# Optimization experiments

Measured on AMD Instinct MI355X. Metric: run time of the kernel, lower is better.

Reference implementation:

```python
import jax
import jax.numpy as jnp
from jax import lax
import numpy as np

EPS = 1e-5
CLASS_COUNT = 1000

# conv specs: (out_c, in_c, k, pool_stride)
_SPECS = [(8, 1, 11, 1), (32, 8, 7, 2), (64, 32, 5, 2), (64, 64, 5, 2), (128, 64, 5, 2), (128, 128, 3, 2)]


def _maxpool3(x, stride):
    return lax.reduce_window(x, -jnp.inf, lax.max, (1, 1, 3, 3), (1, 1, stride, stride), 'VALID')


def _block(x, w, gamma, beta, pool_stride):
    # tanh soft-binarized weights (mode=1, w=1)
    wq = jnp.tanh(w)
    y = lax.conv_general_dilated(x, wq, (1, 1), 'VALID', dimension_numbers=('NCHW', 'OIHW', 'NCHW'))
    y = _maxpool3(y, pool_stride)
    # BatchNorm2d in training mode: batch statistics over (N,H,W), biased var
    mu = jnp.mean(y, axis=(0, 2, 3), keepdims=True)
    var = jnp.var(y, axis=(0, 2, 3), keepdims=True)
    y = (y - mu) * lax.rsqrt(var + EPS)
    y = y * gamma.reshape(1, -1, 1, 1) + beta.reshape(1, -1, 1, 1)
    # tanh soft-binarized activation (mode=1, w=1)
    return jnp.tanh(y)


def setup_inputs() -> dict:
    key = jax.random.key(0)
    keys = jax.random.split(key, 8)
    inp = {'x': jax.random.normal(keys[0], (128, 1, 227, 227), dtype=jnp.float32)}
    for i, (oc, ic, k, _) in enumerate(_SPECS):
        fan_in = ic * k * k
        inp[f'w{i+1}'] = jax.random.normal(keys[i + 1], (oc, ic, k, k), dtype=jnp.float32) / np.sqrt(fan_in)
        inp[f'g{i+1}'] = jnp.ones((oc,), dtype=jnp.float32)
        inp[f'b{i+1}'] = jnp.zeros((oc,), dtype=jnp.float32)
    inp['wl'] = jax.random.normal(keys[7], (CLASS_COUNT, 512), dtype=jnp.float32) / np.sqrt(512.0)
    return inp


def reference(x, w1, w2, w3, w4, w5, w6, g1, g2, g3, g4, g5, g6,
              b1, b2, b3, b4, b5, b6, wl):
    ws = (w1, w2, w3, w4, w5, w6)
    gs = (g1, g2, g3, g4, g5, g6)
    bs = (b1, b2, b3, b4, b5, b6)
    for i, (_, _, _, ps) in enumerate(_SPECS):
        x = _block(x, ws[i], gs[i], bs[i], ps)
    # flatten -> BinaryLinear (tanh-binarized weight, no bias)
    x = x.reshape(x.shape[0], -1)  # [B, 512]
    return x @ jnp.tanh(wl).T  # [B, classCount]
```

## Files before the change

### kernel.cpp

```cpp
#include <hip/hip_runtime.h>
#include <hip/hip_bf16.h>
#include <hip/hip_fp16.h>

using bf16 = __hip_bfloat16;
using f16  = _Float16;
using f16x8 = __attribute__((ext_vector_type(8))) _Float16;
using f32x4  = __attribute__((ext_vector_type(4))) float;
typedef unsigned long long u64;

__device__ __forceinline__ float b2f(bf16 v){ return __bfloat162float(v); }
__device__ __forceinline__ bf16 f2b(float v){ return __float2bfloat16(v); }
__device__ __forceinline__ float ldf(const float* p){ return *p; }
__device__ __forceinline__ float ldf(const bf16* p){ return b2f(*p); }
__device__ __forceinline__ float ldf(const __half* p){ return __half2float(*p); }
__device__ __forceinline__ void stf(float* p, float v){ *p = v; }
__device__ __forceinline__ void stf(bf16* p, float v){ *p = f2b(v); }
__device__ __forceinline__ void stf(__half* p, float v){ *p = __float2half(v); }

__global__ void detect_dtype(const void* __restrict__ g1, int* __restrict__ flag)
{
    if (blockIdx.x == 0 && threadIdx.x == 0)
        *flag = (*(const unsigned*)g1 == 0x3F803F80u) ? 1 : 0;
}

__device__ __forceinline__ float ld_any(const void* p, int i, int isBf16)
{
    return isBf16 ? b2f(((const bf16*)p)[i]) : ((const float*)p)[i];
}

__global__ void xconv(const void* __restrict__ xin, float* __restrict__ xf,
                      const int* __restrict__ flag, int n)
{
    int bf = *flag;
    int i = blockIdx.x * blockDim.x + threadIdx.x;
    if (i < n) xf[i] = ld_any(xin, i, bf);
}

__global__ void wq_tanh(const void* __restrict__ w, float* __restrict__ wq,
                        const int* __restrict__ flag, int n)
{
    int bf = *flag;
    int i = blockIdx.x * blockDim.x + threadIdx.x;
    if (i < n) wq[i] = tanhf(ld_any(w, i, bf));
}

__global__ void wl_transform(const void* __restrict__ wl, float* __restrict__ wlqT,
                             const int* __restrict__ flag)
{
    int bf = *flag;
    int i = blockIdx.x * blockDim.x + threadIdx.x;
    if (i < 1000 * 512) {
        int cls = i >> 9;
        int k   = i & 511;
        wlqT[k * 1000 + cls] = tanhf(ld_any(wl, i, bf));
    }
}

__global__ void wprep_b2(const void* __restrict__ w2, const int* __restrict__ flag,
                         __half* __restrict__ wpk)
{
    int bf = *flag;
    int i = blockIdx.x * 256 + threadIdx.x;
    if (i >= 13728) return;
    int pair = i / 264;
    int slot = i - pair * 264;
    __half v = __float2half(0.f);
    if (pair < 49 && slot < 256) {
        int oc = slot >> 3, ic = slot & 7;
        v = __float2half(tanhf(ld_any(w2, (oc * 8 + ic) * 49 + pair, bf)));
    }
    wpk[i] = v;
}

__global__ void wprep_b3(const void* __restrict__ w3, const int* __restrict__ flag,
                         __half* __restrict__ wpk3)
{
    int bf = *flag;
    int i = blockIdx.x * 256 + threadIdx.x;
    if (i >= 51200) return;
    int tap = i >> 11;
    int g   = (i >> 9) & 3;
    int col = (i >> 5) & 15;
    int icp = i & 31;
    int oc  = g * 16 + col;
    wpk3[i] = __float2half(tanhf(ld_any(w3, (oc * 32 + icp) * 25 + tap, bf)));
}

__global__ void wprep_b4(const void* __restrict__ w4, const int* __restrict__ flag,
                         __half* __restrict__ wpk4)
{
    int bf = *flag;
    int i = blockIdx.x * 256 + threadIdx.x;
    if (i >= 102400) return;
    int step = i >> 11;
    int g    = (i >> 9) & 3;
    int col  = (i >> 5) & 15;
    int icp  = i & 31;
    int icg  = step / 25, tap = step - icg * 25;
    int oc   = g * 16 + col;
    int ic   = icg * 32 + icp;
    wpk4[i] = __float2half(tanhf(ld_any(w4, (oc * 64 + ic) * 25 + tap, bf)));
}

__global__ void wprep_b5(const void* __restrict__ w5, const int* __restrict__ flag,
                         __half* __restrict__ wpk5)
{
    int bf = *flag;
    int i = blockIdx.x * 256 + threadIdx.x;
    if (i >= 204800) return;
    int step = i >> 12;
    int ocg  = (i >> 11) & 1;
    int g    = (i >> 9) & 3;
    int col  = (i >> 5) & 15;
    int icp  = i & 31;
    int icg  = step / 25, tap = step - icg * 25;
    int oc   = ocg * 64 + g * 16 + col;
    int ic   = icg * 32 + icp;
    wpk5[i] = __float2half(tanhf(ld_any(w5, (oc * 64 + ic) * 25 + tap, bf)));
}

template<int CBITS>
__global__ __launch_bounds__(256)
void bn_apply8(const __half* raw, __half* out, const float* __restrict__ ss, int n8)
{
    int i = blockIdx.x * 256 + threadIdx.x;
    if (i >= n8) return;
    f16x8 v = *(const f16x8*)((const f16*)raw + (size_t)i * 8);
    int c0 = (i * 8) & ((1 << CBITS) - 1);
    f16x8 o;
    #pragma unroll
    for (int j = 0; j < 8; j++) {
        int c = c0 + j;
        o[j] = (f16)tanhf(fmaf((float)v[j], ss[c], ss[(1 << CBITS) + c]));
    }
    *(f16x8*)((f16*)out + (size_t)i * 8) = o;
}

__global__ __launch_bounds__(256)
void b2conv(const __half* __restrict__ A1, const __half* __restrict__ wpk,
            __half* __restrict__ raw, float* __restrict__ sums)
{
    constexpr int WPS = 264;

    __shared__ __align__(16) char smem[32000];
    __shared__ float s_part[512];
    f16*   xs = (f16*)smem;
    float* pb = (float*)smem;

    const int tid = threadIdx.x;
    const int n   = blockIdx.z;
    const int ty  = blockIdx.x / 15, tx = blockIdx.x - ty * 15;
    const int cy0 = ty * 30, cx0 = tx * 14;

    for (int i = tid; i < 836; i += 256) {
        int r = i / 22, c = i - r * 22;
        int gr = cy0 + r, gc = cx0 + c;
        u64 v0 = 0, v1 = 0;
        if (gr < 215 && gc < 215) {
            const u64* src = (const u64*)(A1 + ((size_t)(n * 215 + gr) * 215 + gc) * 8);
            v0 = src[0]; v1 = src[1];
        }
        u64* dst = (u64*)(xs + i * 8);
        dst[0] = v0; dst[1] = v1;
    }
    __syncthreads();

    const int lane = tid & 63, wid = tid >> 6;
    const int col = lane & 15, q = lane >> 4;

    int aoff[13];
    #pragma unroll
    for (int s = 0; s < 13; s++) {
        int pp = s * 4 + q;
        int kh = (pp < 49) ? pp / 7 : 0;
        int kw = (pp < 49) ? pp - (pp / 7) * 7 : 0;
        aoff[s] = kh * 22 + kw;
    }

    f32x4 acc[8][2];
    #pragma unroll
    for (int f = 0; f < 8; f++)
        #pragma unroll
        for (int g = 0; g < 2; g++)
            acc[f][g] = (f32x4){0.f, 0.f, 0.f, 0.f};

    const f16* wb = (const f16*)wpk + q * WPS + col * 8;
    f16x8 wc0 = *(const f16x8*)(wb);
    f16x8 wc1 = *(const f16x8*)(wb + 128);

    #pragma unroll
    for (int s = 0; s < 13; s++) {
        f16x8 wn0 = wc0, wn1 = wc1;
        if (s < 12) {
            const f16* wn = (const f16*)wpk + ((s + 1) * 4 + q) * WPS + col * 8;
            wn0 = *(const f16x8*)(wn);
            wn1 = *(const f16x8*)(wn + 128);
        }
        #pragma unroll
        for (int f = 0; f < 8; f++) {
            int gi = (wid * 8 + f) * 22 + col + aoff[s];
            f16x8 a = *(const f16x8*)(xs + gi * 8);
            acc[f][0] = __builtin_amdgcn_mfma_f32_16x16x32_f16(a, wc0, acc[f][0], 0, 0, 0);
            acc[f][1] = __builtin_amdgcn_mfma_f32_16x16x32_f16(a, wc1, acc[f][1], 0, 0, 0);
        }
        wc0 = wn0; wc1 = wn1;
    }
    __syncthreads();

    for (int h = 0; h < 2; h++) {
        #pragma unroll
        for (int f = 0; f < 8; f++) {
            int cr = wid * 8 + f;
            if (cr < 31)
                *(f32x4*)(pb + col * 500 + cr * 16 + q * 4) = acc[f][h];
        }
        __syncthreads();
        const int ocl = tid >> 4, slot = tid & 15;
        float sm = 0.f, sq = 0.f;
        for (int j = slot; j < 105; j += 16) {
            int py = j / 7, px = j - (j / 7) * 7;
            int gph = ty * 15 + py, gpw = tx * 7 + px;
            if (gph < 104 && gpw < 104) {
                const float* cp = pb + ocl * 500 + (2 * py) * 16 + 2 * px;
                float m = cp[0];
                #pragma unroll
                for (int dy = 0; dy < 3; dy++)
                    #pragma unroll
                    for (int dx = 0; dx < 3; dx++)
                        m = fmaxf(m, cp[dy * 16 + dx]);
                int oc = h * 16 + ocl;
                size_t oidx = ((size_t)(n * 104 + gph) * 104 + gpw) * 32 + oc;
                raw[oidx] = __float2half(m);
                sm += m; sq += m * m;
            }
        }
        s_part[tid] = sm; s_part[256 + tid] = sq;
        __syncthreads();
        if (tid < 16) {
            float a = 0.f, b = 0.f;
            #pragma unroll
            for (int t = 0; t < 16; t++) {
                a += s_part[tid * 16 + t];
                b += s_part[256 + tid * 16 + t];
            }
            atomicAdd(&sums[h * 16 + tid],      a);
            atomicAdd(&sums[32 + h * 16 + tid], b);
        }
        __syncthreads();
    }
}

__global__ __launch_bounds__(256)
void b3conv(const __half* __restrict__ A2, const __half* __restrict__ wpk3,
            float* __restrict__ A3, float* __restrict__ sums)
{
    __shared__ __align__(16) char smem[32000];
    __shared__ float s_part[512];
    f16*   xs = (f16*)smem;
    float* pb = (float*)smem;

    const int tid = threadIdx.x;
    const int n   = blockIdx.z;
    const int ty  = blockIdx.x / 7, tx = blockIdx.x - ty * 7;
    const int y0  = ty * 14, x0 = tx * 14;

    for (int i = tid; i < 1600; i += 256) {
        int pos = i >> 2, g8 = i & 3;
        int gy = y0 + pos / 20, gx = x0 + pos % 20;
        *(f16x8*)(xs + pos * 40 + g8 * 8) =
            *(const f16x8*)((const f16*)A2 + ((size_t)(n * 104 + gy) * 104 + gx) * 32 + g8 * 8);
    }

    const int lane = tid & 63, wid = tid >> 6;
    const int col = lane & 15, q = lane >> 4;

    f32x4 acc[4][4];
    #pragma unroll
    for (int f = 0; f < 4; f++)
        #pragma unroll
        for (int g = 0; g < 4; g++)
            acc[f][g] = (f32x4){0.f, 0.f, 0.f, 0.f};

    const f16* wb = (const f16*)wpk3 + col * 32 + q * 8;
    f16x8 w[4];
    #pragma unroll
    for (int g = 0; g < 4; g++)
        w[g] = *(const f16x8*)(wb + g * 512);

    __syncthreads();

    #pragma unroll 1
    for (int tap = 0; tap < 25; tap++) {
        const f16* wnb = wb + (tap < 24 ? tap + 1 : tap) * 2048;
        f16x8 wn[4];
        #pragma unroll
        for (int g = 0; g < 4; g++)
            wn[g] = *(const f16x8*)(wnb + g * 512);

        int kh = tap / 5, kw = tap - (tap / 5) * 5;
        f16x8 a[4];
        #pragma unroll
        for (int f = 0; f < 4; f++) {
            int pos = (wid * 4 + f + kh) * 20 + col + kw;
            a[f] = *(const f16x8*)(xs + pos * 40 + q * 8);
        }
        #pragma unroll
        for (int g = 0; g < 4; g++)
            #pragma unroll
            for (int f = 0; f < 4; f++)
                acc[f][g] = __builtin_amdgcn_mfma_f32_16x16x32_f16(
                    a[f], w[g], acc[f][g], 0, 0, 0);
        #pragma unroll
        for (int g = 0; g < 4; g++)
            w[g] = wn[g];
    }

    for (int h = 0; h < 2; h++) {
        __syncthreads();
        #pragma unroll
        for (int f = 0; f < 4; f++) {
            int cr = wid * 4 + f;
            if (cr < 15) {
                #pragma unroll
                for (int gg = 0; gg < 2; gg++)
                    *(f32x4*)(pb + (gg * 16 + col) * 244 + cr * 16 + q * 4) = acc[f][h * 2 + gg];
            }
        }
        __syncthreads();
        const int ocl = tid >> 3, slot = tid & 7;
        float sm = 0.f, sq = 0.f;
        for (int j = slot; j < 49; j += 8) {
            int py = j / 7, px = j - (j / 7) * 7;
            const float* cp = pb + ocl * 244 + (2 * py) * 16 + 2 * px;
            float m = cp[0];
            #pragma unroll
            for (int dy = 0; dy < 3; dy++)
                #pragma unroll
                for (int dx = 0; dx < 3; dx++)
                    m = fmaxf(m, cp[dy * 16 + dx]);
            A3[((size_t)(n * 64 + h * 32 + ocl) * 49 + ty * 7 + py) * 49 + tx * 7 + px] = m;
            sm += m; sq += m * m;
        }
        s_part[tid] = sm; s_part[256 + tid] = sq;
        __syncthreads();
        if (tid < 32) {
            float a = 0.f, b = 0.f;
            #pragma unroll
            for (int t = 0; t < 8; t++) {
                a += s_part[tid * 8 + t];
                b += s_part[256 + tid * 8 + t];
            }
            atomicAdd(&sums[h * 32 + tid],      a);
            atomicAdd(&sums[64 + h * 32 + tid], b);
        }
    }
}

__global__ __launch_bounds__(256)
void bn_tanh_h_t(const float* __restrict__ x, const float* __restrict__ ss,
                 __half* __restrict__ out)
{
    __shared__ float tile[64][50];
    const int tid = threadIdx.x;
    const int h = blockIdx.x % 49;
    const int n = blockIdx.x / 49;
    const int c = tid >> 2, j = tid & 3;
    const float* xp = x + ((size_t)(n * 64 + c) * 49 + h) * 49;
    for (int w = j; w < 49; w += 4)
        tile[c][w] = xp[w];
    __syncthreads();
    __half* op = out + ((size_t)(n * 49 + h) * 49) * 64;
    for (int pos = tid; pos < 49 * 64; pos += 256) {
        int w = pos >> 6, cc = pos & 63;
        op[pos] = __float2half(tanhf(fmaf(tile[cc][w], ss[cc], ss[64 + cc])));
    }
}

__global__ __launch_bounds__(256)
void bn4_apply(const float* __restrict__ x, const float* __restrict__ ss,
               __half* __restrict__ out)
{
    int idx = blockIdx.x * 256 + threadIdx.x;
    if (idx >= 3964928) return;
    int w  = idx % 22;
    int t1 = idx / 22;
    int h  = t1 % 22;
    int t2 = t1 / 22;
    int c  = t2 & 63;
    int n  = t2 >> 6;
    float t = tanhf(fmaf(x[idx], ss[c], ss[64 + c]));
    out[((size_t)(n * 22 + h) * 22 + w) * 64 + c] = __float2half(t);
}

__global__ __launch_bounds__(256)
void b4conv(const __half* __restrict__ A3t, const __half* __restrict__ wpk4,
            float* __restrict__ A4, float* __restrict__ sums)
{
    __shared__ __align__(16) char smem[31232];
    __shared__ float s_part[512];
    f16*   xs = (f16*)smem;
    float* pb = (float*)smem;

    const int tid = threadIdx.x;
    const int n   = blockIdx.z;
    const int ty  = blockIdx.x >> 2, tx = blockIdx.x & 3;
    const int y0  = ty * 14, x0 = tx * 14;
    const int lane = tid & 63, wid = tid >> 6;
    const int col = lane & 15, q = lane >> 4;

    f32x4 acc[4][4];
    #pragma unroll
    for (int f = 0; f < 4; f++)
        #pragma unroll
        for (int g = 0; g < 4; g++)
            acc[f][g] = (f32x4){0.f, 0.f, 0.f, 0.f};

    const f16* wb = (const f16*)wpk4 + col * 32 + q * 8;
    f16x8 w[4];
    #pragma unroll
    for (int g = 0; g < 4; g++)
        w[g] = *(const f16x8*)(wb + g * 512);

    #pragma unroll 1
    for (int icg = 0; icg < 2; icg++) {
        __syncthreads();
        for (int i = tid; i < 1520; i += 256) {
            int pos = i >> 2, g8 = i & 3;
            int gy = y0 + pos / 20, gx = x0 + pos % 20;
            f16x8 v = (f16x8){0, 0, 0, 0, 0, 0, 0, 0};
            if (gy < 49 && gx < 49)
                v = *(const f16x8*)((const f16*)A3t +
                    ((size_t)(n * 49 + gy) * 49 + gx) * 64 + icg * 32 + g8 * 8);
            *(f16x8*)(xs + pos * 40 + g8 * 8) = v;
        }
        __syncthreads();

        #pragma unroll 1
        for (int tap = 0; tap < 25; tap++) {
            int step = icg * 25 + tap;
            const f16* wnb = wb + (size_t)(step < 49 ? step + 1 : step) * 2048;
            f16x8 wn[4];
            #pragma unroll
            for (int g = 0; g < 4; g++)
                wn[g] = *(const f16x8*)(wnb + g * 512);

            int kh = tap / 5, kw = tap - (tap / 5) * 5;
            f16x8 a[4];
            #pragma unroll
            for (int f = 0; f < 4; f++) {
                int r = wid * 4 + f + kh; if (r > 18) r = 18;
                int pos = r * 20 + col + kw;
                a[f] = *(const f16x8*)(xs + pos * 40 + q * 8);
            }
            #pragma unroll
            for (int g = 0; g < 4; g++)
                #pragma unroll
                for (int f = 0; f < 4; f++)
                    acc[f][g] = __builtin_amdgcn_mfma_f32_16x16x32_f16(
                        a[f], w[g], acc[f][g], 0, 0, 0);
            #pragma unroll
            for (int g = 0; g < 4; g++)
                w[g] = wn[g];
        }
    }

    for (int h = 0; h < 2; h++) {
        __syncthreads();
        #pragma unroll
        for (int f = 0; f < 4; f++) {
            int cr = wid * 4 + f;
            if (cr < 15) {
                #pragma unroll
                for (int gg = 0; gg < 2; gg++)
                    *(f32x4*)(pb + (gg * 16 + col) * 244 + cr * 16 + q * 4) = acc[f][h * 2 + gg];
            }
        }
        __syncthreads();
        const int ocl = tid >> 3, slot = tid & 7;
        float sm = 0.f, sq = 0.f;
        for (int j = slot; j < 49; j += 8) {
            int py = j / 7, px = j - (j / 7) * 7;
            int gph = ty * 7 + py, gpw = tx * 7 + px;
            if (gph < 22 && gpw < 22) {
                const float* cp = pb + ocl * 244 + (2 * py) * 16 + 2 * px;
                float m = cp[0];
                #pragma unroll
                for (int dy = 0; dy < 3; dy++)
                    #pragma unroll
                    for (int dx = 0; dx < 3; dx++)
                        m = fmaxf(m, cp[dy * 16 + dx]);
                A4[((size_t)(n * 64 + h * 32 + ocl) * 22 + gph) * 22 + gpw] = m;
                sm += m; sq += m * m;
            }
        }
        s_part[tid] = sm; s_part[256 + tid] = sq;
        __syncthreads();
        if (tid < 32) {
            float a = 0.f, b = 0.f;
            #pragma unroll
            for (int t = 0; t < 8; t++) {
                a += s_part[tid * 8 + t];
                b += s_part[256 + tid * 8 + t];
            }
            atomicAdd(&sums[h * 32 + tid],      a);
            atomicAdd(&sums[64 + h * 32 + tid], b);
        }
    }
}

__global__ __launch_bounds__(256)
void b5conv(const __half* __restrict__ A4t, const __half* __restrict__ wpk5,
            float* __restrict__ A5, float* __restrict__ sums)
{
    __shared__ __align__(16) char smem[49664];
    __shared__ float s_part[512];
    f16*   xs = (f16*)smem;
    float* pb = (float*)smem;

    const int tid = threadIdx.x;
    const int n   = blockIdx.z;
    const int ocg = blockIdx.x;
    const int lane = tid & 63, wid = tid >> 6;
    const int col = lane & 15, q = lane >> 4;

    int abase[6];
    #pragma unroll
    for (int f = 0; f < 6; f++) {
        int m = (wid * 6 + f) * 16 + col;
        if (m > 323) m = 323;
        int r = m / 18, cc = m - r * 18;
        abase[f] = r * 22 + cc;
    }

    f32x4 acc[6][4];
    #pragma unroll
    for (int f = 0; f < 6; f++)
        #pragma unroll
        for (int g = 0; g < 4; g++)
            acc[f][g] = (f32x4){0.f, 0.f, 0.f, 0.f};

    const f16* wb = (const f16*)wpk5 + ocg * 2048 + col * 32 + q * 8;
    f16x8 w[4];
    #pragma unroll
    for (int g = 0; g < 4; g++)
        w[g] = *(const f16x8*)(wb + g * 512);

    #pragma unroll 1
    for (int icg = 0; icg < 2; icg++) {
        __syncthreads();
        for (int i = tid; i < 1936; i += 256) {
            int pos = i >> 2, g8 = i & 3;
            *(f16x8*)(xs + pos * 40 + g8 * 8) =
                *(const f16x8*)((const f16*)A4t + ((size_t)(n * 484 + pos)) * 64
                                + icg * 32 + g8 * 8);
        }
        __syncthreads();

        #pragma unroll 1
        for (int tap = 0; tap < 25; tap++) {
            int step = icg * 25 + tap;
            const f16* wnb = wb + (size_t)(step < 49 ? step + 1 : step) * 4096;
            f16x8 wn[4];
            #pragma unroll
            for (int g = 0; g < 4; g++)
                wn[g] = *(const f16x8*)(wnb + g * 512);

            int kh = tap / 5, kw = tap - (tap / 5) * 5;
            int off = kh * 22 + kw;
            f16x8 a[6];
            #pragma unroll
            for (int f = 0; f < 6; f++)
                a[f] = *(const f16x8*)(xs + (abase[f] + off) * 40 + q * 8);
            #pragma unroll
            for (int g = 0; g < 4; g++)
                #pragma unroll
                for (int f = 0; f < 6; f++)
                    acc[f][g] = __builtin_amdgcn_mfma_f32_16x16x32_f16(
                        a[f], w[g], acc[f][g], 0, 0, 0);
            #pragma unroll
            for (int g = 0; g < 4; g++)
                w[g] = wn[g];
        }
    }

    for (int h = 0; h < 2; h++) {
        __syncthreads();
        #pragma unroll
        for (int f = 0; f < 6; f++)
            #pragma unroll
            for (int gg = 0; gg < 2; gg++)
                *(f32x4*)(pb + (gg * 16 + col) * 388 + (wid * 6 + f) * 16 + q * 4)
                    = acc[f][h * 2 + gg];
        __syncthreads();
        const int ocl = tid >> 3, slot = tid & 7;
        float sm = 0.f, sq = 0.f;
        for (int j = slot; j < 64; j += 8) {
            int py = j >> 3, px = j & 7;
            const float* cp = pb + ocl * 388 + (2 * py) * 18 + 2 * px;
            float m = cp[0];
            #pragma unroll
            for (int dy = 0; dy < 3; dy++)
                #pragma unroll
                for (int dx = 0; dx < 3; dx++)
                    m = fmaxf(m, cp[dy * 18 + dx]);
            int oc = ocg * 64 + h * 32 + ocl;
            A5[((size_t)(n * 128 + oc) * 8 + py) * 8 + px] = m;
            sm += m; sq += m * m;
        }
        s_part[tid] = sm; s_part[256 + tid] = sq;
        __syncthreads();
        if (tid < 32) {
            float a = 0.f, b = 0.f;
            #pragma unroll
            for (int t = 0; t < 8; t++) {
                a += s_part[tid * 8 + t];
                b += s_part[256 + tid * 8 + t];
            }
            int oc = ocg * 64 + h * 32 + tid;
            atomicAdd(&sums[oc],       a);
            atomicAdd(&sums[128 + oc], b);
        }
    }
}

template<int MODE, int IC, int OC, int K, int PS, int TPH, int TPW,
         int OCB, int OCT, int CIC, int NP, bool ONHWC, typename InT, typename OutT>
__global__ __launch_bounds__(256)
void ctile(const InT* __restrict__ in, const float* __restrict__ wq,
           OutT* __restrict__ out, float* __restrict__ sums,
           const float* __restrict__ ss,
           int Hin, int Win, int PH, int PW, int tilesX)
{
    constexpr int TPO  = OCB / OCT;
    constexpr int CH   = PS * (TPH - 1) + 3;
    constexpr int CW   = PS * (TPW - 1) + 3;
    constexpr int SPR  = (CW + NP - 1) / NP;
    constexpr int CWP  = SPR * NP;
    constexpr int NSTR = CH * SPR;
    static_assert(NSTR * TPO <= 256, "thread mapping overflow");
    constexpr int IH   = CH + K - 1;
    constexpr int IW   = CW + K - 1;
    constexpr int IWE_ = (CWP + K - 1 > IW) ? (CWP + K - 1) : IW;
    constexpr int IWE  = IWE_ | 1;
    constexpr int IN_SZ  = CIC * IH * IWE;
    constexpr int INP    = (IN_SZ + 3) & ~3;
    constexpr int W_SZ   = CIC * K * K * OCB;
    constexpr int CONV_SZ = OCB * CH * CWP;
    constexpr int LDS_SZ = (INP + W_SZ > CONV_SZ) ? (INP + W_SZ) : CONV_SZ;

    __shared__ __align__(16) float lds[LDS_SZ];
    __shared__ float s_part[512];

    const int tid = threadIdx.x;
    const int n   = blockIdx.z;
    const int oc0 = blockIdx.y * OCB;
    const int tY  = blockIdx.x / tilesX;
    const int tX  = blockIdx.x - tY * tilesX;
    const int ph0 = tY * TPH, pw0 = tX * TPW;
    const int ih0 = ph0 * PS, iw0 = pw0 * PS;

    const int  og  = tid % TPO;
    const int  s   = tid / TPO;
    const bool act = (s < NSTR);
    const int  r   = s / SPR;
    const int  c0  = (s - r * SPR) * NP;

    float acc[NP][OCT];
    #pragma unroll
    for (int p = 0; p < NP; p++)
        #pragma unroll
        for (int o = 0; o < OCT; o++) acc[p][o] = 0.f;

    for (int icb = 0; icb < IC; icb += CIC) {
        for (int idx = tid; idx < IN_SZ; idx += 256) {
            int ic  = idx / (IH * IWE);
            int rem = idx - ic * (IH * IWE);
            int rr  = rem / IWE, cc = rem - rr * IWE;
            int gr  = ih0 + rr, gc = iw0 + cc;
            float v = 0.f;
            if (gr < Hin && gc < Win)
                v = ldf(&in[((size_t)(n * IC + icb + ic) * Hin + gr) * Win + gc]);
            lds[idx] = v;
        }
        for (int idx = tid; idx < W_SZ; idx += 256) {
            int ocl = idx % OCB;
            int kk  = (idx / OCB) % (K * K);
            int c_  = idx / (OCB * K * K);
            lds[INP + idx] = wq[((size_t)(oc0 + ocl) * IC + icb + c_) * (K * K) + kk];
        }
        __syncthreads();

        if (act) {
            #pragma unroll 1
            for (int ic_ = 0; ic_ < CIC; ic_++) {
                const float* xb = lds + ic_ * (IH * IWE);
                const float* wb = lds + INP + ic_ * (K * K * OCB) + og * OCT;
                #pragma unroll 1
                for (int kh = 0; kh < K; kh++) {
                    const float* xr = xb + (r + kh) * IWE + c0;
                    float xwin[NP + K - 1];
                    #pragma unroll
                    for (int j = 0; j < NP + K - 1; j++) xwin[j] = xr[j];
                    #pragma unroll
                    for (int kw = 0; kw < K; kw++) {
                        const float* wp2 = wb + (kh * K + kw) * OCB;
                        float wv[OCT];
                        #pragma unroll
                        for (int o = 0; o < OCT; o += 4) {
                            float4 t = *(const float4*)(wp2 + o);
                            wv[o] = t.x; wv[o+1] = t.y; wv[o+2] = t.z; wv[o+3] = t.w;
                        }
                        #pragma unroll
                        for (int p = 0; p < NP; p++)
                            #pragma unroll
                            for (int o = 0; o < OCT; o++)
                                acc[p][o] = fmaf(wv[o], xwin[p + kw], acc[p][o]);
                    }
                }
            }
        }
        __syncthreads();
    }

    if (act) {
        #pragma unroll
        for (int p = 0; p < NP; p++)
            #pragma unroll
            for (int o = 0; o < OCT; o++)
                lds[(og * OCT + o) * (CH * CWP) + r * CWP + c0 + p] = acc[p][o];
    }
    __syncthreads();

    {
        constexpr int TPC = 256 / OCB;
        const int ocl = tid / TPC, slot = tid - ocl * TPC;
        float sm = 0.f, sq = 0.f;
        for (int j = slot; j < TPH * TPW; j += TPC) {
            int py = j / TPW, px = j - (j / TPW) * TPW;
            int gph = ph0 + py, gpw = pw0 + px;
            if (gph < PH && gpw < PW) {
                const float* cp = lds + ocl * (CH * CWP) + (py * PS) * CWP + px * PS;
                float m = cp[0];
                #pragma unroll
                for (int dy = 0; dy < 3; dy++)
                    #pragma unroll
                    for (int dx = 0; dx < 3; dx++)
                        m = fmaxf(m, cp[dy * CWP + dx]);
                size_t oidx = ONHWC
                    ? ((size_t)(n * PH + gph) * PW + gpw) * OC + oc0 + ocl
                    : ((size_t)(n * OC + oc0 + ocl) * PH + gph) * PW + gpw;
                if (MODE == 2) {
                    int c = oc0 + ocl;
                    stf(&out[oidx], tanhf(fmaf(m, ss[c], ss[OC + c])));
                } else {
                    if (MODE == 0) stf(&out[oidx], m);
                    sm += m; sq += m * m;
                }
            }
        }
        if (MODE != 2) {
            s_part[tid] = sm; s_part[256 + tid] = sq;
            __syncthreads();
            if (tid < OCB) {
                float a = 0.f, b = 0.f;
                #pragma unroll
                for (int t = 0; t < TPC; t++) {
                    a += s_part[tid * TPC + t];
                    b += s_part[256 + tid * TPC + t];
                }
                atomicAdd(&sums[oc0 + tid],      a);
                atomicAdd(&sums[OC + oc0 + tid], b);
            }
        }
    }
}

template<int K, int APPLY, typename InT, typename OutT>
__global__ __launch_bounds__(256)
void convpool(const InT* __restrict__ in, const float* __restrict__ wq,
              OutT* __restrict__ out, const float* __restrict__ ss,
              int IC, int OC, int PS, int Hin, int Win, int PH, int PW, int total)
{
    for (int idx = blockIdx.x * 256 + threadIdx.x; idx < total;
         idx += gridDim.x * 256) {
        int pw = idx % PW;
        int t1 = idx / PW;
        int ph = t1 % PH;
        int t2 = t1 / PH;
        int oc = t2 % OC;
        int n  = t2 / OC;
        const int by = ph * PS, bx = pw * PS;

        float acc[3][3];
        #pragma unroll
        for (int a = 0; a < 3; a++)
            #pragma unroll
            for (int b = 0; b < 3; b++) acc[a][b] = 0.f;

        const float* wp = wq + oc * IC * K * K;
        const InT*   np = in + (n * IC) * Hin * Win;

        #pragma unroll 1
        for (int ic = 0; ic < IC; ic++) {
            const InT*   xp = np + ic * Hin * Win;
            const float* wc = wp + ic * K * K;
            #pragma unroll
            for (int r = 0; r < K + 2; r++) {
                float xr[K + 2];
                const InT* xrow = xp + (by + r) * Win + bx;
                #pragma unroll
                for (int j = 0; j < K + 2; j++) xr[j] = ldf(&xrow[j]);
                #pragma unroll
                for (int dy = 0; dy < 3; dy++) {
                    const int kh = r - dy;
                    if (0 <= kh && kh < K) {
                        const float* wrow = wc + kh * K;
                        #pragma unroll
                        for (int kw = 0; kw < K; kw++) {
                            float w = wrow[kw];
                            acc[dy][0] = fmaf(w, xr[kw + 0], acc[dy][0]);
                            acc[dy][1] = fmaf(w, xr[kw + 1], acc[dy][1]);
                            acc[dy][2] = fmaf(w, xr[kw + 2], acc[dy][2]);
                        }
                    }
                }
            }
        }
        float m = acc[0][0];
        #pragma unroll
        for (int a = 0; a < 3; a++)
            #pragma unroll
            for (int b = 0; b < 3; b++) m = fmaxf(m, acc[a][b]);
        if (APPLY) m = tanhf(fmaf(m, ss[oc], ss[OC + oc]));
        stf(&out[idx], m);
    }
}

template<typename T>
__global__ __launch_bounds__(256)
void stats_k(const T* __restrict__ x, float* __restrict__ sums,
             int N, int C, int PHW, int bpc)
{
    int c   = blockIdx.x / bpc;
    int sub = blockIdx.x % bpc;
    int perC = N * PHW;
    float s = 0.f, s2 = 0.f;
    for (int j = sub * 256 + threadIdx.x; j < perC; j += bpc * 256) {
        int n = j / PHW, p = j - n * PHW;
        float v = ldf(&x[(n * C + c) * PHW + p]);
        s += v; s2 += v * v;
    }
    __shared__ float ls[256], ls2[256];
    ls[threadIdx.x] = s; ls2[threadIdx.x] = s2;
    __syncthreads();
    for (int w = 128; w > 0; w >>= 1) {
        if (threadIdx.x < w) {
            ls[threadIdx.x]  += ls[threadIdx.x + w];
            ls2[threadIdx.x] += ls2[threadIdx.x + w];
        }
        __syncthreads();
    }
    if (threadIdx.x == 0) {
        atomicAdd(&sums[c],     ls[0]);
        atomicAdd(&sums[C + c], ls2[0]);
    }
}

__global__ void bn_prep(const float* __restrict__ sums, const void* __restrict__ g,
                        const void* __restrict__ b, const int* __restrict__ flag,
                        float* __restrict__ ss, int C, float invCnt)
{
    int bf = *flag;
    int c = blockIdx.x * blockDim.x + threadIdx.x;
    if (c < C) {
        float mean = sums[c] * invCnt;
        float var  = sums[C + c] * invCnt - mean * mean;
        float rstd = rsqrtf(fmaxf(var, 0.f) + 1e-5f);
        float sc   = ld_any(g, c, bf) * rstd;
        ss[c]      = sc;
        ss[C + c]  = ld_any(b, c, bf) - mean * sc;
    }
}

__global__ __launch_bounds__(256)
void bn_tanh(float* __restrict__ x, const float* __restrict__ ss, int C, int PHW)
{
    int plane = blockIdx.y;
    int c = plane & (C - 1);
    float sc = ss[c], sh = ss[C + c];
    float* xp = x + (long)plane * PHW;
    for (int i = blockIdx.x * 256 + threadIdx.x; i < PHW; i += 256 * gridDim.x)
        xp[i] = tanhf(fmaf(xp[i], sc, sh));
}

__global__ __launch_bounds__(256)
void linear_k(const float* __restrict__ act, const float* __restrict__ wlqT,
              void* __restrict__ out, const int* __restrict__ flag)
{
    __shared__ float s_a[512];
    int bf = *flag;
    int n = blockIdx.y;
    for (int i = threadIdx.x; i < 512; i += 256) s_a[i] = act[n * 512 + i];
    __syncthreads();
    int cls = blockIdx.x * 256 + threadIdx.x;
    if (cls < 1000) {
        float acc = 0.f;
        #pragma unroll 8
        for (int k = 0; k < 512; k++)
            acc = fmaf(s_a[k], wlqT[k * 1000 + cls], acc);
        if (bf) ((bf16*)out)[n * 1000 + cls] = f2b(acc);
        else    ((float*)out)[n * 1000 + cls] = acc;
    }
}

extern "C" void kernel_launch(void* const* d_in, const int* in_sizes, int n_in,
                              void* d_out, int out_size, void* d_ws, size_t ws_size,
                              hipStream_t stream)
{
    (void)in_sizes; (void)n_in; (void)out_size; (void)ws_size;
    const void* x = d_in[0];
    const void* W[6]; const void* G[6]; const void* B[6];
    for (int i = 0; i < 6; i++) {
        W[i] = d_in[1 + 3 * i];
        G[i] = d_in[2 + 3 * i];
        B[i] = d_in[3 + 3 * i];
    }
    const void* wl = d_in[19];

    char* p = (char*)d_ws;
    auto carve = [&](size_t bytes) -> void* {
        void* r = (void*)p;
        p += (bytes + 255) & ~((size_t)255);
        return r;
    };
    int*   flag = (int*)carve(256);
    const int wsz[6] = {968, 12544, 51200, 102400, 204800, 147456};
    float* wq[6];
    for (int i = 0; i < 6; i++) wq[i] = (float*)carve((size_t)wsz[i] * 4);
    float* wlqT = (float*)carve((size_t)512000 * 4);
    float* sums = (float*)carve(256 * 4);
    float* ss   = (float*)carve(256 * 4);
    __half* wpk  = (__half*)carve((size_t)13728 * 2);
    __half* wpk3 = (__half*)carve((size_t)51200 * 2);
    __half* wpk4 = (__half*)carve((size_t)102400 * 2);
    __half* wpk5 = (__half*)carve((size_t)204800 * 2);
    float* xf   = (float*)carve((size_t)6595712 * 4);
    __half* A1  = (__half*)carve((size_t)47334400 * 2);
    __half* A2  = (__half*)carve((size_t)44302336 * 2);
    float*  A3  = (float*)A1;
    __half* A3t = (__half*)A2;
    float*  A4  = (float*)A1;
    float*  A5  = (float*)A2;
    __half* A4t = (__half*)((char*)A2 + (size_t)16 * 1024 * 1024);
    float*  A6  = (float*)A1;

    auto cdiv = [](int a, int b) { return (a + b - 1) / b; };

    detect_dtype<<<1, 64, 0, stream>>>(G[0], flag);
    xconv<<<cdiv(6595712, 256), 256, 0, stream>>>(x, xf, flag, 6595712);
    wq_tanh<<<cdiv(wsz[0], 256), 256, 0, stream>>>(W[0], wq[0], flag, wsz[0]);
    wq_tanh<<<cdiv(wsz[5], 256), 256, 0, stream>>>(W[5], wq[5], flag, wsz[5]);
    wl_transform<<<cdiv(512000, 256), 256, 0, stream>>>(wl, wlqT, flag);
    wprep_b2<<<cdiv(13728, 256), 256, 0, stream>>>(W[1], flag, wpk);
    wprep_b3<<<cdiv(51200, 256), 256, 0, stream>>>(W[2], flag, wpk3);
    wprep_b4<<<cdiv(102400, 256), 256, 0, stream>>>(W[3], flag, wpk4);
    wprep_b5<<<cdiv(204800, 256), 256, 0, stream>>>(W[4], flag, wpk5);

    hipMemsetAsync(sums, 0, 2 * 8 * 4, stream);
    ctile<0, 1, 8, 11, 1, 34, 40, 8, 8, 1, 7, true, float, __half>
        <<<dim3(42, 1, 128), 256, 0, stream>>>(xf, wq[0], A1, sums, ss, 227, 227, 215, 215, 6);
    bn_prep<<<1, 256, 0, stream>>>(sums, G[0], B[0], flag, ss, 8, 1.f / 5916800.f);
    bn_apply8<3><<<cdiv(5916800, 256), 256, 0, stream>>>(A1, A1, ss, 5916800);

    hipMemsetAsync(sums, 0, 2 * 32 * 4, stream);
    b2conv<<<dim3(105, 1, 128), 256, 0, stream>>>(A1, wpk, A2, sums);
    bn_prep<<<1, 256, 0, stream>>>(sums, G[1], B[1], flag, ss, 32, 1.f / 1384448.f);
    bn_apply8<5><<<cdiv(5537792, 256), 256, 0, stream>>>(A2, A2, ss, 5537792);

    hipMemsetAsync(sums, 0, 2 * 64 * 4, stream);
    b3conv<<<dim3(49, 1, 128), 256, 0, stream>>>(A2, wpk3, A3, sums);
    bn_prep<<<1, 256, 0, stream>>>(sums, G[2], B[2], flag, ss, 64, 1.f / 307328.f);
    bn_tanh_h_t<<<128 * 49, 256, 0, stream>>>(A3, ss, A3t);

    hipMemsetAsync(sums, 0, 2 * 64 * 4, stream);
    b4conv<<<dim3(16, 1, 128), 256, 0, stream>>>(A3t, wpk4, A4, sums);
    bn_prep<<<1, 256, 0, stream>>>(sums, G[3], B[3], flag, ss, 64, 1.f / 61952.f);
    bn4_apply<<<cdiv(3964928, 256), 256, 0, stream>>>(A4, ss, A4t);

    hipMemsetAsync(sums, 0, 2 * 128 * 4, stream);
    b5conv<<<dim3(2, 1, 128), 256, 0, stream>>>(A4t, wpk5, A5, sums);
    bn_prep<<<1, 256, 0, stream>>>(sums, G[4], B[4], flag, ss, 128, 1.f / 8192.f);
    bn_tanh<<<dim3(1, 16384), 256, 0, stream>>>(A5, ss, 128, 64);

    {
        int total = 65536;
        convpool<3, 0, float, float><<<cdiv(total, 256), 256, 0, stream>>>(
            A5, wq[5], A6, ss, 128, 128, 2, 8, 8, 2, 2, total);
        hipMemsetAsync(sums, 0, 2 * 128 * 4, stream);
        stats_k<float><<<128, 256, 0, stream>>>(A6, sums, 128, 128, 4, 1);
        bn_prep<<<1, 256, 0, stream>>>(sums, G[5], B[5], flag, ss, 128, 1.f / 512.f);
        bn_tanh<<<dim3(1, 16384), 256, 0, stream>>>(A6, ss, 128, 4);
    }
    linear_k<<<dim3(4, 128), 256, 0, stream>>>(A6, wlqT, d_out, flag);
}
```

Baseline: 1.512 ms.

## Fuse BN-tanh apply into b2/b3 conv tile loads and relayout b2 weights

Removes the standalone bn_apply8 passes after layers 1 and 2 by applying the batch-norm scale/shift and tanh while staging input tiles into shared memory in b2conv and b3conv. The b2 weight packing is reorganized into kh-group by kw steps, which simplifies the per-step A offsets. This avoids two full read-write passes over large fp16 activations at the cost of recomputing tanh on halo elements and one extra MFMA step in b2conv.

After: 1.483 ms. No clear change (-1.9%).

```diff
diff --git a/kernel.cpp b/kernel.cpp
--- a/kernel.cpp
+++ b/kernel.cpp
@@ -61,14 +61,18 @@
 {
     int bf = *flag;
     int i = blockIdx.x * 256 + threadIdx.x;
-    if (i >= 13728) return;
-    int pair = i / 264;
-    int slot = i - pair * 264;
+    if (i >= 14336) return;
+    int ic  = i & 7;
+    int q   = (i >> 3) & 3;
+    int col = (i >> 5) & 15;
+    int g   = (i >> 9) & 1;
+    int khg = (i >> 10) & 1;
+    int kw  = i >> 11;
+    int kh  = khg * 4 + q;
+    int oc  = g * 16 + col;
     __half v = __float2half(0.f);
-    if (pair < 49 && slot < 256) {
-        int oc = slot >> 3, ic = slot & 7;
-        v = __float2half(tanhf(ld_any(w2, (oc * 8 + ic) * 49 + pair, bf)));
-    }
+    if (kh < 7)
+        v = __float2half(tanhf(ld_any(w2, (oc * 8 + ic) * 49 + kh * 7 + kw, bf)));
     wpk[i] = v;
 }
 
@@ -119,29 +123,11 @@
     wpk5[i] = __float2half(tanhf(ld_any(w5, (oc * 64 + ic) * 25 + tap, bf)));
 }
 
-template<int CBITS>
-__global__ __launch_bounds__(256)
-void bn_apply8(const __half* raw, __half* out, const float* __restrict__ ss, int n8)
-{
-    int i = blockIdx.x * 256 + threadIdx.x;
-    if (i >= n8) return;
-    f16x8 v = *(const f16x8*)((const f16*)raw + (size_t)i * 8);
-    int c0 = (i * 8) & ((1 << CBITS) - 1);
-    f16x8 o;
-    #pragma unroll
-    for (int j = 0; j < 8; j++) {
-        int c = c0 + j;
-        o[j] = (f16)tanhf(fmaf((float)v[j], ss[c], ss[(1 << CBITS) + c]));
-    }
-    *(f16x8*)((f16*)out + (size_t)i * 8) = o;
-}
-
 __global__ __launch_bounds__(256)
 void b2conv(const __half* __restrict__ A1, const __half* __restrict__ wpk,
-            __half* __restrict__ raw, float* __restrict__ sums)
-{
-    constexpr int WPS = 264;
-
+            __half* __restrict__ raw, float* __restrict__ sums,
+            const float* __restrict__ ss)
+{
     __shared__ __align__(16) char smem[32000];
     __shared__ float s_part[512];
     f16*   xs = (f16*)smem;
@@ -152,30 +138,27 @@
     const int ty  = blockIdx.x / 15, tx = blockIdx.x - ty * 15;
     const int cy0 = ty * 30, cx0 = tx * 14;
 
-    for (int i = tid; i < 836; i += 256) {
+    float ssc[8], ssh[8];
+    #pragma unroll
+    for (int j = 0; j < 8; j++) { ssc[j] = ss[j]; ssh[j] = ss[8 + j]; }
+
+    for (int i = tid; i < 858; i += 256) {
         int r = i / 22, c = i - r * 22;
         int gr = cy0 + r, gc = cx0 + c;
-        u64 v0 = 0, v1 = 0;
-        if (gr < 215 && gc < 215) {
-            const u64* src = (const u64*)(A1 + ((size_t)(n * 215 + gr) * 215 + gc) * 8);
-            v0 = src[0]; v1 = src[1];
-        }
-        u64* dst = (u64*)(xs + i * 8);
-        dst[0] = v0; dst[1] = v1;
+        f16x8 v = (f16x8){0, 0, 0, 0, 0, 0, 0, 0};
+        if (gr < 215 && gc < 215)
+            v = *(const f16x8*)((const f16*)A1 + ((size_t)(n * 215 + gr) * 215 + gc) * 8);
+        f16x8 o;
+        #pragma unroll
+        for (int j = 0; j < 8; j++)
+            o[j] = (f16)tanhf(fmaf((float)v[j], ssc[j], ssh[j]));
+        *(f16x8*)(xs + i * 8) = o;
     }
     __syncthreads();
 
     const int lane = tid & 63, wid = tid >> 6;
     const int col = lane & 15, q = lane >> 4;
-
-    int aoff[13];
-    #pragma unroll
-    for (int s = 0; s < 13; s++) {
-        int pp = s * 4 + q;
-        int kh = (pp < 49) ? pp / 7 : 0;
-        int kw = (pp < 49) ? pp - (pp / 7) * 7 : 0;
-        aoff[s] = kh * 22 + kw;
-    }
+    const int arow = q * 22;
 
     f32x4 acc[8][2];
     #pragma unroll
@@ -184,21 +167,23 @@
         for (int g = 0; g < 2; g++)
             acc[f][g] = (f32x4){0.f, 0.f, 0.f, 0.f};
 
-    const f16* wb = (const f16*)wpk + q * WPS + col * 8;
+    const f16* wb = (const f16*)wpk + col * 32 + q * 8;
     f16x8 wc0 = *(const f16x8*)(wb);
-    f16x8 wc1 = *(const f16x8*)(wb + 128);
-
-    #pragma unroll
-    for (int s = 0; s < 13; s++) {
+    f16x8 wc1 = *(const f16x8*)(wb + 512);
+
+    #pragma unroll
+    for (int s = 0; s < 14; s++) {
         f16x8 wn0 = wc0, wn1 = wc1;
-        if (s < 12) {
-            const f16* wn = (const f16*)wpk + ((s + 1) * 4 + q) * WPS + col * 8;
+        if (s < 13) {
+            const f16* wn = wb + (s + 1) * 1024;
             wn0 = *(const f16x8*)(wn);
-            wn1 = *(const f16x8*)(wn + 128);
-        }
+            wn1 = *(const f16x8*)(wn + 512);
+        }
+        int kw = s >> 1, khg = s & 1;
+        int aoffs = arow + khg * 88 + kw;
         #pragma unroll
         for (int f = 0; f < 8; f++) {
-            int gi = (wid * 8 + f) * 22 + col + aoff[s];
+            int gi = (wid * 8 + f) * 22 + col + aoffs;
             f16x8 a = *(const f16x8*)(xs + gi * 8);
             acc[f][0] = __builtin_amdgcn_mfma_f32_16x16x32_f16(a, wc0, acc[f][0], 0, 0, 0);
             acc[f][1] = __builtin_amdgcn_mfma_f32_16x16x32_f16(a, wc1, acc[f][1], 0, 0, 0);
@@ -252,7 +237,8 @@
 
 __global__ __launch_bounds__(256)
 void b3conv(const __half* __restrict__ A2, const __half* __restrict__ wpk3,
-            float* __restrict__ A3, float* __restrict__ sums)
+            float* __restrict__ A3, float* __restrict__ sums,
+            const float* __restrict__ ss)
 {
     __shared__ __align__(16) char smem[32000];
     __shared__ float s_part[512];
@@ -267,8 +253,14 @@
     for (int i = tid; i < 1600; i += 256) {
         int pos = i >> 2, g8 = i & 3;
         int gy = y0 + pos / 20, gx = x0 + pos % 20;
-        *(f16x8*)(xs + pos * 40 + g8 * 8) =
-            *(const f16x8*)((const f16*)A2 + ((size_t)(n * 104 + gy) * 104 + gx) * 32 + g8 * 8);
+        f16x8 v = *(const f16x8*)((const f16*)A2 +
+                  ((size_t)(n * 104 + gy) * 104 + gx) * 32 + g8 * 8);
+        int c0 = g8 * 8;
+        f16x8 o;
+        #pragma unroll
+        for (int j = 0; j < 8; j++)
+            o[j] = (f16)tanhf(fmaf((float)v[j], ss[c0 + j], ss[32 + c0 + j]));
+        *(f16x8*)(xs + pos * 40 + g8 * 8) = o;
     }
 
     const int lane = tid & 63, wid = tid >> 6;
@@ -940,7 +932,7 @@
     float* wlqT = (float*)carve((size_t)512000 * 4);
     float* sums = (float*)carve(256 * 4);
     float* ss   = (float*)carve(256 * 4);
-    __half* wpk  = (__half*)carve((size_t)13728 * 2);
+    __half* wpk  = (__half*)carve((size_t)14336 * 2);
     __half* wpk3 = (__half*)carve((size_t)51200 * 2);
     __half* wpk4 = (__half*)carve((size_t)102400 * 2);
     __half* wpk5 = (__half*)carve((size_t)204800 * 2);
@@ -961,7 +953,7 @@
     wq_tanh<<<cdiv(wsz[0], 256), 256, 0, stream>>>(W[0], wq[0], flag, wsz[0]);
     wq_tanh<<<cdiv(wsz[5], 256), 256, 0, stream>>>(W[5], wq[5], flag, wsz[5]);
     wl_transform<<<cdiv(512000, 256), 256, 0, stream>>>(wl, wlqT, flag);
-    wprep_b2<<<cdiv(13728, 256), 256, 0, stream>>>(W[1], flag, wpk);
+    wprep_b2<<<cdiv(14336, 256), 256, 0, stream>>>(W[1], flag, wpk);
     wprep_b3<<<cdiv(51200, 256), 256, 0, stream>>>(W[2], flag, wpk3);
     wprep_b4<<<cdiv(102400, 256), 256, 0, stream>>>(W[3], flag, wpk4);
     wprep_b5<<<cdiv(204800, 256), 256, 0, stream>>>(W[4], flag, wpk5);
@@ -970,15 +962,13 @@
     ctile<0, 1, 8, 11, 1, 34, 40, 8, 8, 1, 7, true, float, __half>
         <<<dim3(42, 1, 128), 256, 0, stream>>>(xf, wq[0], A1, sums, ss, 227, 227, 215, 215, 6);
     bn_prep<<<1, 256, 0, stream>>>(sums, G[0], B[0], flag, ss, 8, 1.f / 5916800.f);
-    bn_apply8<3><<<cdiv(5916800, 256), 256, 0, stream>>>(A1, A1, ss, 5916800);
 
     hipMemsetAsync(sums, 0, 2 * 32 * 4, stream);
-    b2conv<<<dim3(105, 1, 128), 256, 0, stream>>>(A1, wpk, A2, sums);
+    b2conv<<<dim3(105, 1, 128), 256, 0, stream>>>(A1, wpk, A2, sums, ss);
     bn_prep<<<1, 256, 0, stream>>>(sums, G[1], B[1], flag, ss, 32, 1.f / 1384448.f);
-    bn_apply8<5><<<cdiv(5537792, 256), 256, 0, stream>>>(A2, A2, ss, 5537792);
 
     hipMemsetAsync(sums, 0, 2 * 64 * 4, stream);
-    b3conv<<<dim3(49, 1, 128), 256, 0, stream>>>(A2, wpk3, A3, sums);
+    b3conv<<<dim3(49, 1, 128), 256, 0, stream>>>(A2, wpk3, A3, sums, ss);
     bn_prep<<<1, 256, 0, stream>>>(sums, G[2], B[2], flag, ss, 64, 1.f / 307328.f);
     bn_tanh_h_t<<<128 * 49, 256, 0, stream>>>(A3, ss, A3t);
 
```
